# Kernel optimization log

Measured on AMD Instinct MI355X. Metric: run time of the kernel, lower is better.

## Reference

```python
import jax, jax.numpy as jnp
import numpy as np

B, S, D_IN, E = 64, 199, 1024, 256
INNER, K = 512, 4
NH_M, DH_M = 4, 128
NH_S, DH_S = 4, 64
FF_UP = 384
SLSTM_AT = (1, 4)


def layernorm(x, w, eps=1e-5):
    mu = x.mean(-1, keepdims=True)
    var = x.var(-1, keepdims=True)
    return (x - mu) * jax.lax.rsqrt(var + eps) * w


def mh_layernorm(h, w, eps=1e-5):
    # h: (B,S,NH,DH): normalize per head over DH, scale by w (NH*DH,)
    mu = h.mean(-1, keepdims=True)
    var = h.var(-1, keepdims=True)
    hn = (h - mu) * jax.lax.rsqrt(var + eps)
    b, s, nh, dh = h.shape
    return hn.reshape(b, s, nh * dh) * w


def causal_conv(x, w, b):
    # depthwise causal conv; x (B,S,C), w (C,K), b (C,)
    k = w.shape[-1]
    s = x.shape[1]
    xp = jnp.pad(x, ((0, 0), (k - 1, 0), (0, 0)))
    y = sum(xp[:, i:i + s, :] * w[:, i] for i in range(k))
    return y + b


def headwise(x, w):
    # block-diagonal linear (LinearHeadwiseExpand): x (B,S,H*d), w (H,o,d)
    b, s, _ = x.shape
    h, o, d = w.shape
    y = jnp.einsum('bshd,hod->bsho', x.reshape(b, s, h, d), w)
    return y.reshape(b, s, h * o)


def mlstm_parallel(q, k, v, ig, fg):
    # stabilized parallel mLSTM; q,k,v (B,NH,S,DH); ig,fg (B,NH,S)
    s, dh = q.shape[2], q.shape[3]
    logf = jax.nn.log_sigmoid(fg)
    lfc = jnp.cumsum(logf, axis=-1)
    lfc = jnp.concatenate([jnp.zeros_like(lfc[..., :1]), lfc], axis=-1)  # (B,NH,S+1)
    mat = lfc[..., :, None] - lfc[..., None, :]
    mask = jnp.tril(jnp.ones((s + 1, s + 1), dtype=bool))
    mat = jnp.where(mask, mat, -jnp.inf)
    logD = mat[..., 1:, 1:] + ig[..., None, :]            # (B,NH,S,S)
    maxD = jnp.max(logD, axis=-1, keepdims=True)
    Dm = jnp.exp(logD - maxD)
    qk = jnp.einsum('bnsd,bntd->bnst', q, k) / (dh ** 0.5)
    C = qk * Dm
    norm = jnp.maximum(jnp.abs(C.sum(-1, keepdims=True)), jnp.exp(-maxD))
    return jnp.einsum('bnst,bntd->bnsd', C / (norm + 1e-6), v)


def mlstm_layer(x, proj_up, conv_w, conv_b, q_w, k_w, v_w, ig_w, ig_b, fg_w, fg_b, skip, outnorm_w, proj_down):
    b, s, _ = x.shape
    xi = x @ proj_up                                      # (B,S,2*INNER)
    x_m, z = jnp.split(xi, 2, axis=-1)
    xca = jax.nn.silu(causal_conv(x_m, conv_w, conv_b))
    q = headwise(xca, q_w)
    k = headwise(xca, k_w)
    v = headwise(x_m, v_w)
    gate_in = jnp.concatenate([q, k, v], axis=-1)         # (B,S,3*INNER)
    ig = (gate_in @ ig_w.T + ig_b).transpose(0, 2, 1)     # (B,NH,S)
    fg = (gate_in @ fg_w.T + fg_b).transpose(0, 2, 1)
    qh = q.reshape(b, s, NH_M, DH_M).transpose(0, 2, 1, 3)
    kh = k.reshape(b, s, NH_M, DH_M).transpose(0, 2, 1, 3)
    vh = v.reshape(b, s, NH_M, DH_M).transpose(0, 2, 1, 3)
    h = mlstm_parallel(qh, kh, vh, ig, fg)                # (B,NH,S,DH)
    hn = mh_layernorm(h.transpose(0, 2, 1, 3), outnorm_w) # (B,S,INNER)
    h_state = (hn + skip * xca) * jax.nn.silu(z)
    return h_state @ proj_down


def slstm_layer(x, conv_w, conv_b, gate_w, rec_w, bias, gn_w):
    b, s, _ = x.shape
    xc = jax.nn.silu(causal_conv(x, conv_w, conv_b))
    xch = xc.reshape(b, s, NH_S, DH_S)
    xh = x.reshape(b, s, NH_S, DH_S)
    gi = jnp.einsum('bshd,hod->bsho', xch, gate_w[0])
    gf = jnp.einsum('bshd,hod->bsho', xch, gate_w[1])
    gz = jnp.einsum('bshd,hod->bsho', xh, gate_w[2])
    go = jnp.einsum('bshd,hod->bsho', xh, gate_w[3])
    Wx = jnp.stack([gi, gf, gz, go], axis=2)              # (B,S,4,NH,DH)

    def step(carry, wx):
        h, c, n, m = carry
        raw = wx + jnp.einsum('bhd,ghod->bgho', h, rec_w) + bias
        iraw, fraw, zraw, oraw = raw[:, 0], raw[:, 1], raw[:, 2], raw[:, 3]
        logfplusm = m + jax.nn.log_sigmoid(fraw)
        m_new = jnp.maximum(iraw, logfplusm)
        igate = jnp.exp(iraw - m_new)
        fgate = jnp.exp(logfplusm - m_new)
        c_new = fgate * c + igate * jnp.tanh(zraw)
        n_new = fgate * n + igate
        h_new = jax.nn.sigmoid(oraw) * (c_new / n_new)
        return (h_new, c_new, n_new, m_new), h_new

    z0 = jnp.zeros((b, NH_S, DH_S), x.dtype)
    _, ys = jax.lax.scan(step, (z0, z0, z0, z0), jnp.moveaxis(Wx, 1, 0))
    y = jnp.moveaxis(ys, 0, 1)                            # (B,S,NH,DH)
    return mh_layernorm(y, gn_w)


def gated_ffn(x, w_up, w_dn):
    gate, up = jnp.split(x @ w_up, 2, axis=-1)
    return (jax.nn.gelu(gate) * up) @ w_dn


def forward_fn(x, w_down, b_down, m_ln_w, m_proj_up, m_conv_w, m_conv_b, m_q_w, m_k_w, m_v_w,
               m_ig_w, m_ig_b, m_fg_w, m_fg_b, m_skip, m_outnorm_w, m_proj_down,
               s_ln_w, s_conv_w, s_conv_b, s_gate_w, s_rec_w, s_bias, s_gn_w, s_ln2_w,
               s_ffn_up, s_ffn_down, post_ln_w, w_emo, b_emo, w_sen, b_sen):
    h = x @ w_down + b_down                               # (B,S,E)
    mi = si = 0
    for blk in range(7):
        if blk in SLSTM_AT:
            h = h + slstm_layer(layernorm(h, s_ln_w[si]), s_conv_w[si], s_conv_b[si],
                                s_gate_w[si], s_rec_w[si], s_bias[si], s_gn_w[si])
            h = h + gated_ffn(layernorm(h, s_ln2_w[si]), s_ffn_up[si], s_ffn_down[si])
            si += 1
        else:
            h = h + mlstm_layer(layernorm(h, m_ln_w[mi]), m_proj_up[mi], m_conv_w[mi], m_conv_b[mi],
                                m_q_w[mi], m_k_w[mi], m_v_w[mi], m_ig_w[mi], m_ig_b[mi],
                                m_fg_w[mi], m_fg_b[mi], m_skip[mi], m_outnorm_w[mi], m_proj_down[mi])
            mi += 1
    h = jax.nn.selu(layernorm(h, post_ln_w))
    pooled = h.mean(axis=1)                               # (B,E)
    return pooled @ w_emo + b_emo, pooled @ w_sen + b_sen


def setup_inputs() -> dict:
    ks = iter(jax.random.split(jax.random.key(0), 40))
    def p(*shape, s=0.02):
        return jax.random.normal(next(ks), shape, dtype=jnp.float32) * s
    inp = dict(
        x=jax.random.normal(next(ks), (B, S, D_IN), dtype=jnp.float32),
        w_down=p(D_IN, E), b_down=jnp.zeros((E,), jnp.float32),
        m_ln_w=jnp.ones((5, E), jnp.float32),
        m_proj_up=p(5, E, 2 * INNER),
        m_conv_w=p(5, INNER, K), m_conv_b=jnp.zeros((5, INNER), jnp.float32),
        m_q_w=p(5, 128, 4, 4), m_k_w=p(5, 128, 4, 4), m_v_w=p(5, 128, 4, 4),
        m_ig_w=p(5, NH_M, 3 * INNER), m_ig_b=p(5, NH_M, s=0.1),
        m_fg_w=p(5, NH_M, 3 * INNER),
        m_fg_b=jnp.tile(jnp.linspace(3.0, 6.0, NH_M, dtype=jnp.float32), (5, 1)),
        m_skip=jnp.ones((5, INNER), jnp.float32),
        m_outnorm_w=jnp.ones((5, INNER), jnp.float32),
        m_proj_down=p(5, INNER, E),
        s_ln_w=jnp.ones((2, E), jnp.float32),
        s_conv_w=p(2, E, K), s_conv_b=jnp.zeros((2, E), jnp.float32),
        s_gate_w=p(2, 4, NH_S, DH_S, DH_S),
        s_rec_w=p(2, 4, NH_S, DH_S, DH_S),
        s_bias=jnp.zeros((2, 4, NH_S, DH_S), jnp.float32).at[:, 1].set(3.0),
        s_gn_w=jnp.ones((2, E), jnp.float32),
        s_ln2_w=jnp.ones((2, E), jnp.float32),
        s_ffn_up=p(2, E, 2 * FF_UP), s_ffn_down=p(2, FF_UP, E),
        post_ln_w=jnp.ones((E,), jnp.float32),
        w_emo=p(E, 7), b_emo=jnp.zeros((7,), jnp.float32),
        w_sen=p(E, 3), b_sen=jnp.zeros((3,), jnp.float32),
    )
    return inp


def reference(x, w_down, b_down, m_ln_w, m_proj_up, m_conv_w, m_conv_b, m_q_w, m_k_w, m_v_w,
              m_ig_w, m_ig_b, m_fg_w, m_fg_b, m_skip, m_outnorm_w, m_proj_down,
              s_ln_w, s_conv_w, s_conv_b, s_gate_w, s_rec_w, s_bias, s_gn_w, s_ln2_w,
              s_ffn_up, s_ffn_down, post_ln_w, w_emo, b_emo, w_sen, b_sen):
    return forward_fn(x, w_down, b_down, m_ln_w, m_proj_up, m_conv_w, m_conv_b, m_q_w, m_k_w, m_v_w,
                      m_ig_w, m_ig_b, m_fg_w, m_fg_b, m_skip, m_outnorm_w, m_proj_down,
                      s_ln_w, s_conv_w, s_conv_b, s_gate_w, s_rec_w, s_bias, s_gn_w, s_ln2_w,
                      s_ffn_up, s_ffn_down, post_ln_w, w_emo, b_emo, w_sen, b_sen)
```

## Files before the change

### kernel.cpp

```cpp
#include <hip/hip_runtime.h>
#include <hip/hip_bf16.h>
#include <math.h>


#define B_    64
#define S_    199
#define E_    256
#define NTOK  (B_*S_)
#define NQT   13

typedef __attribute__((ext_vector_type(8))) short short8;
typedef __attribute__((ext_vector_type(4))) float floatx4;
typedef unsigned short ushort_t;

__device__ __forceinline__ float sigmoidf_(float x) { return 1.f / (1.f + expf(-x)); }
__device__ __forceinline__ float siluf_(float x) { return x / (1.f + expf(-x)); }
__device__ __forceinline__ float logsigf_(float x) { return fminf(x, 0.f) - log1pf(expf(-fabsf(x))); }

__device__ __forceinline__ ushort_t f2b(float f) {
    union { float f; unsigned u; } v; v.f = f;
    unsigned r = (v.u + 0x7fffu + ((v.u >> 16) & 1u)) >> 16;
    return (ushort_t)r;
}
__device__ __forceinline__ float bf2f(ushort_t u) {
    union { unsigned u; float f; } v; v.u = ((unsigned)u) << 16;
    return v.f;
}
__device__ __forceinline__ void unp2(unsigned d, float& lo, float& hi) {
    union { unsigned u; float f; } a, b;
    a.u = d << 16; b.u = d & 0xffff0000u;
    lo = a.f; hi = b.f;
}

__global__ void cvt_bf(const float* __restrict__ in, ushort_t* __restrict__ out, int n4) {
    int i = blockIdx.x * 256 + threadIdx.x;
    if (i >= n4) return;
    float4 v = *(const float4*)&in[i * 4];
    union { ushort_t us[4]; uint2 u; } t;
    t.us[0] = f2b(v.x); t.us[1] = f2b(v.y); t.us[2] = f2b(v.z); t.us[3] = f2b(v.w);
    *(uint2*)&out[i * 4] = t.u;
}

__global__ void __launch_bounds__(256)
gemm_bf(const ushort_t* __restrict__ A, const ushort_t* __restrict__ Bw,
        const float* __restrict__ bias, float* __restrict__ C,
        int M, int K, int N, int accum) {
    __shared__ __align__(16) ushort_t As[64][40];
    __shared__ __align__(16) ushort_t Bs[128][40];
    int tid = threadIdx.x;
    int wave = tid >> 6, lane = tid & 63;
    int wm = wave >> 1, wn = wave & 1;
    int quad = lane >> 4, l16 = lane & 15;
    int m0 = blockIdx.y * 64, n0 = blockIdx.x * 128;
    floatx4 zero = {0.f, 0.f, 0.f, 0.f};
    floatx4 acc[2][4];
    #pragma unroll
    for (int i = 0; i < 2; i++)
        #pragma unroll
        for (int j = 0; j < 4; j++) acc[i][j] = zero;
    int ar = tid >> 2, ac = (tid & 3) * 8;
    int bn = tid & 127, bkg = (tid >> 7) * 16;
    for (int k0 = 0; k0 < K; k0 += 32) {
        *(uint4*)&As[ar][ac] = *(const uint4*)(A + (size_t)(m0 + ar) * K + k0 + ac);
        {
            const ushort_t* bp = Bw + (size_t)(k0 + bkg) * N + n0 + bn;
            union { ushort_t us[16]; uint4 v[2]; } t;
            #pragma unroll
            for (int i = 0; i < 16; i++) t.us[i] = bp[(size_t)i * N];
            *(uint4*)&Bs[bn][bkg] = t.v[0];
            *(uint4*)&Bs[bn][bkg + 8] = t.v[1];
        }
        __syncthreads();
        short8 af[2], bf[4];
        #pragma unroll
        for (int i = 0; i < 2; i++) af[i] = *(const short8*)&As[wm * 32 + i * 16 + l16][quad * 8];
        #pragma unroll
        for (int j = 0; j < 4; j++) bf[j] = *(const short8*)&Bs[wn * 64 + j * 16 + l16][quad * 8];
        #pragma unroll
        for (int i = 0; i < 2; i++)
            #pragma unroll
            for (int j = 0; j < 4; j++)
                acc[i][j] = __builtin_amdgcn_mfma_f32_16x16x32_bf16(af[i], bf[j], acc[i][j], 0, 0, 0);
        __syncthreads();
    }
    #pragma unroll
    for (int i = 0; i < 2; i++)
        #pragma unroll
        for (int j = 0; j < 4; j++)
            #pragma unroll
            for (int r = 0; r < 4; r++) {
                int row = m0 + wm * 32 + i * 16 + quad * 4 + r;
                int col = n0 + wn * 64 + j * 16 + l16;
                float o = acc[i][j][r];
                if (bias) o += bias[col];
                float* cp = &C[(size_t)row * N + col];
                if (accum) o += *cp;
                *cp = o;
            }
}

__global__ void __launch_bounds__(256)
gemm_mfma(const float* __restrict__ A, const float* __restrict__ Bw,
          const float* __restrict__ bias, float* __restrict__ C,
          int M, int K, int N, int accum) {
    __shared__ __align__(16) ushort_t As[64][40];
    __shared__ __align__(16) ushort_t Bs[64][40];
    int tid = threadIdx.x;
    int wave = tid >> 6, lane = tid & 63;
    int wm = wave >> 1, wn = wave & 1;
    int quad = lane >> 4, l16 = lane & 15;
    int m0 = blockIdx.y * 64, n0 = blockIdx.x * 64;
    floatx4 zero = {0.f, 0.f, 0.f, 0.f};
    floatx4 acc[2][2];
    acc[0][0] = zero; acc[0][1] = zero; acc[1][0] = zero; acc[1][1] = zero;
    int ar = tid >> 2, ac = (tid & 3) * 8;
    int bn = tid & 63, bk = (tid >> 6) * 8;
    for (int k0 = 0; k0 < K; k0 += 32) {
        {
            const float* ap = A + (size_t)(m0 + ar) * K + k0 + ac;
            union { ushort_t us[8]; uint4 v; } t;
            #pragma unroll
            for (int i = 0; i < 8; i++) t.us[i] = f2b(ap[i]);
            *(uint4*)&As[ar][ac] = t.v;
        }
        {
            const float* bp = Bw + (size_t)(k0 + bk) * N + n0 + bn;
            union { ushort_t us[8]; uint4 v; } t;
            #pragma unroll
            for (int i = 0; i < 8; i++) t.us[i] = f2b(bp[(size_t)i * N]);
            *(uint4*)&Bs[bn][bk] = t.v;
        }
        __syncthreads();
        short8 af[2], bf[2];
        #pragma unroll
        for (int i = 0; i < 2; i++) af[i] = *(const short8*)&As[wm * 32 + i * 16 + l16][quad * 8];
        #pragma unroll
        for (int j = 0; j < 2; j++) bf[j] = *(const short8*)&Bs[wn * 32 + j * 16 + l16][quad * 8];
        #pragma unroll
        for (int i = 0; i < 2; i++)
            #pragma unroll
            for (int j = 0; j < 2; j++)
                acc[i][j] = __builtin_amdgcn_mfma_f32_16x16x32_bf16(af[i], bf[j], acc[i][j], 0, 0, 0);
        __syncthreads();
    }
    #pragma unroll
    for (int i = 0; i < 2; i++)
        #pragma unroll
        for (int j = 0; j < 2; j++)
            #pragma unroll
            for (int r = 0; r < 4; r++) {
                int row = m0 + wm * 32 + i * 16 + quad * 4 + r;
                int col = n0 + wn * 32 + j * 16 + l16;
                float o = acc[i][j][r];
                if (bias) o += bias[col];
                float* cp = &C[(size_t)row * N + col];
                if (accum) o += *cp;
                *cp = o;
            }
}

__global__ void __launch_bounds__(256)
slstm_wx_mfma(const ushort_t* __restrict__ xc, const ushort_t* __restrict__ xln,
              const float* __restrict__ gw, float* __restrict__ Wx) {
    __shared__ __align__(16) ushort_t As[64][40];
    __shared__ __align__(16) ushort_t Bs[64][40];
    int gh = blockIdx.y; int g = gh >> 2, hh = gh & 3;
    const ushort_t* src = (g < 2) ? xc : xln;
    const float* w = gw + (size_t)gh * 4096;
    int tid = threadIdx.x;
    int wave = tid >> 6, lane = tid & 63;
    int wm = wave >> 1, wn = wave & 1;
    int quad = lane >> 4, l16 = lane & 15;
    int m0 = blockIdx.x * 64;
    floatx4 zero = {0.f, 0.f, 0.f, 0.f};
    floatx4 acc[2][2];
    acc[0][0] = zero; acc[0][1] = zero; acc[1][0] = zero; acc[1][1] = zero;
    int ar = tid >> 2, ac = (tid & 3) * 8;
    int bn = tid & 63, bk = (tid >> 6) * 8;
    #pragma unroll
    for (int kt = 0; kt < 2; kt++) {
        int k0 = kt * 32;
        *(uint4*)&As[ar][ac] = *(const uint4*)(src + (size_t)(m0 + ar) * 256 + hh * 64 + k0 + ac);
        {
            const float* bp = w + (size_t)bn * 64 + k0 + bk;
            union { ushort_t us[8]; uint4 v; } t;
            #pragma unroll
            for (int i = 0; i < 8; i++) t.us[i] = f2b(bp[i]);
            *(uint4*)&Bs[bn][bk] = t.v;
        }
        __syncthreads();
        short8 af[2], bf[2];
        #pragma unroll
        for (int i = 0; i < 2; i++) af[i] = *(const short8*)&As[wm * 32 + i * 16 + l16][quad * 8];
        #pragma unroll
        for (int j = 0; j < 2; j++) bf[j] = *(const short8*)&Bs[wn * 32 + j * 16 + l16][quad * 8];
        #pragma unroll
        for (int i = 0; i < 2; i++)
            #pragma unroll
            for (int j = 0; j < 2; j++)
                acc[i][j] = __builtin_amdgcn_mfma_f32_16x16x32_bf16(af[i], bf[j], acc[i][j], 0, 0, 0);
        __syncthreads();
    }
    #pragma unroll
    for (int i = 0; i < 2; i++)
        #pragma unroll
        for (int j = 0; j < 2; j++)
            #pragma unroll
            for (int r = 0; r < 4; r++) {
                int row = m0 + wm * 32 + i * 16 + quad * 4 + r;
                int col = wn * 32 + j * 16 + l16;
                Wx[(size_t)row * 1024 + g * 256 + hh * 64 + col] = acc[i][j][r];
            }
}

__global__ void __launch_bounds__(256)
layernorm256(const float* __restrict__ x, const float* __restrict__ w, ushort_t* __restrict__ y) {
    int n = blockIdx.x, t = threadIdx.x;
    float v = x[(size_t)n * 256 + t];
    float s = v, s2 = v * v;
    #pragma unroll
    for (int off = 32; off; off >>= 1) { s += __shfl_xor(s, off); s2 += __shfl_xor(s2, off); }
    __shared__ float ps[4], ps2[4];
    if ((t & 63) == 0) { ps[t >> 6] = s; ps2[t >> 6] = s2; }
    __syncthreads();
    float S = ps[0] + ps[1] + ps[2] + ps[3];
    float S2 = ps2[0] + ps2[1] + ps2[2] + ps2[3];
    float mu = S / 256.f, var = S2 / 256.f - mu * mu;
    y[(size_t)n * 256 + t] = f2b((v - mu) * rsqrtf(var + 1e-5f) * w[t]);
}

__global__ void __launch_bounds__(256)
postln_selu(const float* __restrict__ x, const float* __restrict__ w, float* __restrict__ y) {
    int n = blockIdx.x, t = threadIdx.x;
    float v = x[(size_t)n * 256 + t];
    float s = v, s2 = v * v;
    #pragma unroll
    for (int off = 32; off; off >>= 1) { s += __shfl_xor(s, off); s2 += __shfl_xor(s2, off); }
    __shared__ float ps[4], ps2[4];
    if ((t & 63) == 0) { ps[t >> 6] = s; ps2[t >> 6] = s2; }
    __syncthreads();
    float S = ps[0] + ps[1] + ps[2] + ps[3];
    float S2 = ps2[0] + ps2[1] + ps2[2] + ps2[3];
    float mu = S / 256.f, var = S2 / 256.f - mu * mu;
    float yn = (v - mu) * rsqrtf(var + 1e-5f) * w[t];
    y[(size_t)n * 256 + t] = 1.0507009873554805f * (yn > 0.f ? yn : 1.6732632423543772f * (expf(yn) - 1.f));
}

__global__ void __launch_bounds__(256)
fused_qkv(const float* __restrict__ xi, const float* __restrict__ cw,
          const float* __restrict__ cb,
          const float* __restrict__ qw, const float* __restrict__ kw,
          const float* __restrict__ vw,
          float* __restrict__ xca,
          ushort_t* __restrict__ q16, ushort_t* __restrict__ k16, ushort_t* __restrict__ v16) {
    int idx = blockIdx.x * 256 + threadIdx.x;
    if (idx >= NTOK * 128) return;
    int n = idx >> 7, hh = idx & 127;
    int b = n / S_, s = n - b * S_;
    int c0 = hh * 4;
    float4 hist[4];
    #pragma unroll
    for (int i = 0; i < 4; i++) {
        int sp = s - 3 + i;
        if (sp >= 0) hist[i] = *(const float4*)(xi + (size_t)(b * S_ + sp) * 1024 + c0);
        else hist[i] = (float4){0.f, 0.f, 0.f, 0.f};
    }
    float xm[4] = {hist[3].x, hist[3].y, hist[3].z, hist[3].w};
    float xc4[4];
    #pragma unroll
    for (int d = 0; d < 4; d++) {
        float y = cb[c0 + d];
        const float* cwp = cw + (c0 + d) * 4;
        y += hist[0].x * 0.f;
        float hv[4] = { d==0?hist[0].x:(d==1?hist[0].y:(d==2?hist[0].z:hist[0].w)),
                        d==0?hist[1].x:(d==1?hist[1].y:(d==2?hist[1].z:hist[1].w)),
                        d==0?hist[2].x:(d==1?hist[2].y:(d==2?hist[2].z:hist[2].w)),
                        xm[d] };
        #pragma unroll
        for (int i = 0; i < 4; i++) y += hv[i] * cwp[i];
        xc4[d] = siluf_(y);
    }
    *(float4*)(xca + (size_t)n * 512 + c0) = (float4){xc4[0], xc4[1], xc4[2], xc4[3]};
    union { ushort_t us[4]; uint2 u; } qo, ko, vo;
    #pragma unroll
    for (int o = 0; o < 4; o++) {
        const float* qp = qw + (c0 + o) * 4;
        const float* kp = kw + (c0 + o) * 4;
        const float* vp = vw + (c0 + o) * 4;
        float aq = 0.f, ak = 0.f, av = 0.f;
        #pragma unroll
        for (int d = 0; d < 4; d++) {
            aq += xc4[d] * qp[d];
            ak += xc4[d] * kp[d];
            av += xm[d] * vp[d];
        }
        qo.us[o] = f2b(aq); ko.us[o] = f2b(ak); vo.us[o] = f2b(av);
    }
    *(uint2*)(q16 + (size_t)n * 512 + c0) = qo.u;
    *(uint2*)(k16 + (size_t)n * 512 + c0) = ko.u;
    *(uint2*)(v16 + (size_t)n * 512 + c0) = vo.u;
}

__global__ void __launch_bounds__(256)
gates2(const ushort_t* __restrict__ qb, const ushort_t* __restrict__ kb, const ushort_t* __restrict__ vb,
       const float* __restrict__ igw, const float* __restrict__ igbias,
       const float* __restrict__ fgw, const float* __restrict__ fgbias,
       float* __restrict__ igo, float* __restrict__ fgo) {
    int n = blockIdx.x * 4 + (threadIdx.x >> 6);
    int lane = threadIdx.x & 63;
    uint4 q4 = *(const uint4*)(qb + (size_t)n * 512 + lane * 8);
    uint4 k4 = *(const uint4*)(kb + (size_t)n * 512 + lane * 8);
    uint4 v4 = *(const uint4*)(vb + (size_t)n * 512 + lane * 8);
    float q[8], k[8], v[8];
    unp2(q4.x, q[0], q[1]); unp2(q4.y, q[2], q[3]); unp2(q4.z, q[4], q[5]); unp2(q4.w, q[6], q[7]);
    unp2(k4.x, k[0], k[1]); unp2(k4.y, k[2], k[3]); unp2(k4.z, k[4], k[5]); unp2(k4.w, k[6], k[7]);
    unp2(v4.x, v[0], v[1]); unp2(v4.y, v[2], v[3]); unp2(v4.z, v[4], v[5]); unp2(v4.w, v[6], v[7]);
    float acc[8];
    #pragma unroll
    for (int hd = 0; hd < 4; hd++)
        #pragma unroll
        for (int wh = 0; wh < 2; wh++) {
            const float* w = (wh ? fgw : igw) + hd * 1536 + lane * 8;
            float a = 0.f;
            #pragma unroll
            for (int i = 0; i < 8; i++) a += q[i] * w[i];
            #pragma unroll
            for (int i = 0; i < 8; i++) a += k[i] * w[512 + i];
            #pragma unroll
            for (int i = 0; i < 8; i++) a += v[i] * w[1024 + i];
            acc[hd * 2 + wh] = a;
        }
    #pragma unroll
    for (int t = 0; t < 8; t++) {
        float a = acc[t];
        #pragma unroll
        for (int off = 32; off; off >>= 1) a += __shfl_xor(a, off);
        if (lane == 0) {
            int hd = t >> 1, wh = t & 1;
            a += (wh ? fgbias : igbias)[hd];
            (wh ? fgo : igo)[(size_t)n * 4 + hd] = a;
        }
    }
}

__global__ void __launch_bounds__(256)
mlstm_cumsum(const float* __restrict__ fgo, const float* __restrict__ igo,
             float* __restrict__ lfc, float* __restrict__ Mx) {
    int bh = blockIdx.x * 4 + (threadIdx.x >> 6);
    int lane = threadIdx.x & 63;
    int b = bh >> 2, h = bh & 3;
    float v[4]; float lsum = 0.f;
    #pragma unroll
    for (int i = 0; i < 4; i++) {
        int s = lane * 4 + i;
        float f = (s < S_) ? fgo[(size_t)(b * S_ + s) * 4 + h] : 0.f;
        lsum += logsigf_(f);
        v[i] = lsum;
    }
    float x = lsum;
    #pragma unroll
    for (int off = 1; off < 64; off <<= 1) {
        float y = __shfl_up(x, off);
        if (lane >= off) x += y;
    }
    float excl = x - lsum;
    float lf1[4];
    #pragma unroll
    for (int i = 0; i < 4; i++) lf1[i] = excl + v[i];
    if (lane == 0) lfc[bh * (S_ + 1)] = 0.f;
    #pragma unroll
    for (int i = 0; i < 4; i++) {
        int s = lane * 4 + i;
        if (s < S_) lfc[bh * (S_ + 1) + s + 1] = lf1[i];
    }
    float gm[4]; float lmax = -1e30f;
    #pragma unroll
    for (int i = 0; i < 4; i++) {
        int s = lane * 4 + i;
        float ig_ = (s < S_) ? igo[(size_t)(b * S_ + s) * 4 + h] : -1e30f;
        float gg = ig_ - lf1[i];
        lmax = fmaxf(lmax, gg);
        gm[i] = lmax;
    }
    float xm = lmax;
    #pragma unroll
    for (int off = 1; off < 64; off <<= 1) {
        float y = __shfl_up(xm, off);
        if (lane >= off) xm = fmaxf(xm, y);
    }
    float exclm = __shfl_up(xm, 1);
    if (lane == 0) exclm = -1e30f;
    #pragma unroll
    for (int i = 0; i < 4; i++) {
        int s = lane * 4 + i;
        if (s < S_) Mx[bh * S_ + s] = fmaxf(exclm, gm[i]);
    }
}

__global__ void __launch_bounds__(256, 1)
mlstm_attn_mfma(const ushort_t* __restrict__ qb, const ushort_t* __restrict__ kb, const ushort_t* __restrict__ vb,
                const float* __restrict__ igb, const float* __restrict__ lfc, const float* __restrict__ Mx,
                float* __restrict__ outb) {
    __shared__ __align__(16) ushort_t Kb[64 * 136];
    __shared__ __align__(16) ushort_t Vt[128 * 72];
    __shared__ __align__(16) ushort_t Pw[4][16 * 72];
    __shared__ float gv[208], lfv[208], mxv[208];
    int bh = blockIdx.x; int b = bh >> 2, h = bh & 3;
    int tid = threadIdx.x, wave = tid >> 6, lane = tid & 63;
    int quad = lane >> 4, l16 = lane & 15;
    if (tid < 208) {
        if (tid < S_) {
            float lf1 = lfc[bh * (S_ + 1) + tid + 1];
            gv[tid] = igb[(size_t)(b * S_ + tid) * 4 + h] - lf1;
            lfv[tid] = lf1;
            mxv[tid] = Mx[bh * S_ + tid];
        } else { gv[tid] = 0.f; lfv[tid] = 0.f; mxv[tid] = 0.f; }
    }
    floatx4 zero = {0.f, 0.f, 0.f, 0.f};
    float rs[4][4];
    floatx4 accv[4][8];
    #pragma unroll
    for (int qi = 0; qi < 4; qi++) {
        #pragma unroll
        for (int r = 0; r < 4; r++) rs[qi][r] = 0.f;
        #pragma unroll
        for (int dt = 0; dt < 8; dt++) accv[qi][dt] = zero;
    }
    const float scale = 0.08838834764831845f;
    int trow = tid >> 4, d0 = (tid & 15) * 8;
    for (int c = 0; c < 4; c++) {
        __syncthreads();
        #pragma unroll
        for (int i = 0; i < 4; i++) {
            int tl = trow + 16 * i;
            int t = c * 64 + tl;
            union { ushort_t us[8]; uint4 v; } kk, vv;
            if (t < S_) {
                kk.v = *(const uint4*)(kb + (size_t)(b * S_ + t) * 512 + h * 128 + d0);
                vv.v = *(const uint4*)(vb + (size_t)(b * S_ + t) * 512 + h * 128 + d0);
            } else {
                kk.v = (uint4){0, 0, 0, 0};
                vv.v = (uint4){0, 0, 0, 0};
            }
            *(uint4*)&Kb[tl * 136 + d0] = kk.v;
            #pragma unroll
            for (int ii = 0; ii < 8; ii++) Vt[(d0 + ii) * 72 + tl] = vv.us[ii];
        }
        __syncthreads();
        for (int qi = 0; qi < 4; qi++) {
            int qt = wave + 4 * qi;
            if (qt >= NQT || qt < 4 * c) continue;
            uint4 z4 = {0, 0, 0, 0};
            for (int z = lane; z < 144; z += 64) ((uint4*)Pw[wave])[z] = z4;
            int srow = qt * 16 + l16;
            const ushort_t* qp = qb + (size_t)(b * S_ + min(srow, S_ - 1)) * 512 + h * 128 + quad * 8;
            short8 af[4];
            #pragma unroll
            for (int ks = 0; ks < 4; ks++) af[ks] = *(const short8*)(qp + 32 * ks);
            int ktmax_l = min(qt, 4 * c + 3) - 4 * c;
            for (int ktl = 0; ktl <= ktmax_l; ktl++) {
                floatx4 acc = zero;
                #pragma unroll
                for (int ks = 0; ks < 4; ks++) {
                    short8 bf = *(const short8*)&Kb[(ktl * 16 + l16) * 136 + quad * 8 + 32 * ks];
                    acc = __builtin_amdgcn_mfma_f32_16x16x32_bf16(af[ks], bf, acc, 0, 0, 0);
                }
                int tcol = c * 64 + ktl * 16 + l16;
                float gt = gv[tcol];
                #pragma unroll
                for (int r = 0; r < 4; r++) {
                    int s = qt * 16 + quad * 4 + r;
                    bool valid = (tcol <= s) && (tcol < S_);
                    float w = valid ? expf(gt - mxv[s]) : 0.f;
                    float p = acc[r] * scale * w;
                    rs[qi][r] += p;
                    Pw[wave][(quad * 4 + r) * 72 + ktl * 16 + l16] = f2b(p);
                }
            }
            #pragma unroll
            for (int dt = 0; dt < 8; dt++) {
                floatx4 a = accv[qi][dt];
                #pragma unroll
                for (int ks = 0; ks < 2; ks++) {
                    short8 ap = *(const short8*)&Pw[wave][l16 * 72 + quad * 8 + 32 * ks];
                    short8 bp = *(const short8*)&Vt[(dt * 16 + l16) * 72 + quad * 8 + 32 * ks];
                    a = __builtin_amdgcn_mfma_f32_16x16x32_bf16(ap, bp, a, 0, 0, 0);
                }
                accv[qi][dt] = a;
            }
        }
    }
    for (int qi = 0; qi < 4; qi++) {
        int qt = wave + 4 * qi;
        if (qt >= NQT) continue;
        float nrm[4];
        #pragma unroll
        for (int r = 0; r < 4; r++) {
            float v = rs[qi][r];
            v += __shfl_xor(v, 1); v += __shfl_xor(v, 2);
            v += __shfl_xor(v, 4); v += __shfl_xor(v, 8);
            int s = qt * 16 + quad * 4 + r;
            nrm[r] = fmaxf(fabsf(v), expf(-(lfv[s] + mxv[s]))) + 1e-6f;
        }
        #pragma unroll
        for (int dt = 0; dt < 8; dt++)
            #pragma unroll
            for (int r = 0; r < 4; r++) {
                int s = qt * 16 + quad * 4 + r;
                if (s < S_)
                    outb[(size_t)(b * S_ + s) * 512 + h * 128 + dt * 16 + l16] = accv[qi][dt][r] / nrm[r];
            }
    }
}

__global__ void __launch_bounds__(512)
mhln_hstate(const float* __restrict__ hatt, const float* __restrict__ w,
            const float* __restrict__ xca, const float* __restrict__ xi,
            const float* __restrict__ skip, ushort_t* __restrict__ out16) {
    int n = blockIdx.x, t = threadIdx.x;
    float v = hatt[(size_t)n * 512 + t];
    float s = v, s2 = v * v;
    #pragma unroll
    for (int off = 32; off; off >>= 1) { s += __shfl_xor(s, off); s2 += __shfl_xor(s2, off); }
    __shared__ float ps[8], ps2[8];
    if ((t & 63) == 0) { ps[t >> 6] = s; ps2[t >> 6] = s2; }
    __syncthreads();
    int hd = t >> 7;
    float S = ps[hd * 2] + ps[hd * 2 + 1], S2 = ps2[hd * 2] + ps2[hd * 2 + 1];
    float mu = S / 128.f, var = S2 / 128.f - mu * mu;
    float hn = (v - mu) * rsqrtf(var + 1e-5f) * w[t];
    float z = xi[(size_t)n * 1024 + 512 + t];
    out16[(size_t)n * 512 + t] = f2b((hn + skip[t] * xca[(size_t)n * 512 + t]) * siluf_(z));
}

__global__ void conv_silu_s(const ushort_t* __restrict__ xln, const float* __restrict__ cw,
                            const float* __restrict__ cb, ushort_t* __restrict__ xc) {
    int idx = blockIdx.x * blockDim.x + threadIdx.x;
    if (idx >= NTOK * 256) return;
    int n = idx >> 8, c = idx & 255;
    int b = n / S_, s = n - b * S_;
    float y = cb[c];
    #pragma unroll
    for (int i = 0; i < 4; i++) {
        int sp = s - 3 + i;
        if (sp >= 0) y += bf2f(xln[(size_t)(b * S_ + sp) * 256 + c]) * cw[c * 4 + i];
    }
    xc[idx] = f2b(siluf_(y));
}

__global__ void __launch_bounds__(512)
slstm_rec(const float* __restrict__ Wx, const float* __restrict__ rw,
          const float* __restrict__ bias, float* __restrict__ ys) {
    __shared__ __align__(16) float wl[512 * 36];
    __shared__ __align__(16) float hs[64];
    __shared__ float raws[4][64];
    int b = blockIdx.x >> 2, h = blockIdx.x & 3;
    int tid = threadIdx.x;
    int g = tid >> 7, o = (tid >> 1) & 63, kh = tid & 1;
    const float* wp = rw + (size_t)(((g * 4 + h) * 64 + o)) * 64 + kh * 32;
    float* myrow = wl + tid * 36;
    #pragma unroll
    for (int i = 0; i < 8; i++) *(float4*)&myrow[i * 4] = *(const float4*)&wp[i * 4];
    float bi = bias[(g * 4 + h) * 64 + o];
    if (tid < 64) hs[tid] = 0.f;
    float c_ = 0.f, n_ = 0.f, m_ = 0.f;
    size_t wxbase = (size_t)(b * S_) * 1024 + g * 256 + h * 64 + o;
    float wx_cur = Wx[wxbase];
    __syncthreads();
    for (int s = 0; s < S_; s++) {
        float wx_next = (s + 1 < S_) ? Wx[wxbase + (size_t)(s + 1) * 1024] : 0.f;
        float a0 = 0.f, a1 = 0.f, a2 = 0.f, a3 = 0.f;
        #pragma unroll
        for (int d4 = 0; d4 < 8; d4++) {
            float4 wv = *(const float4*)&myrow[d4 * 4];
            float4 hv = *(const float4*)&hs[kh * 32 + d4 * 4];
            a0 += hv.x * wv.x;
            a1 += hv.y * wv.y;
            a2 += hv.z * wv.z;
            a3 += hv.w * wv.w;
        }
        float a = (a0 + a1) + (a2 + a3);
        a += __shfl_xor(a, 1);
        if (kh == 0) raws[g][o] = a + wx_cur + bi;
        __syncthreads();
        float ir = raws[0][o], fr = raws[1][o], zr = raws[2][o], orr = raws[3][o];
        float lfpm = m_ + logsigf_(fr);
        float mn = fmaxf(ir, lfpm);
        float ig = expf(ir - mn), fg = expf(lfpm - mn);
        c_ = fg * c_ + ig * tanhf(zr);
        n_ = fg * n_ + ig;
        m_ = mn;
        float hn = sigmoidf_(orr) * (c_ / n_);
        if (g == 0 && kh == 0) {
            hs[o] = hn;
            ys[(size_t)(b * S_ + s) * 256 + h * 64 + o] = hn;
        }
        __syncthreads();
        wx_cur = wx_next;
    }
}

__global__ void __launch_bounds__(256)
mhln_s_resid(const float* __restrict__ ys, const float* __restrict__ w, float* __restrict__ h) {
    int n = blockIdx.x, t = threadIdx.x;
    float v = ys[(size_t)n * 256 + t];
    float s = v, s2 = v * v;
    #pragma unroll
    for (int off = 32; off; off >>= 1) { s += __shfl_xor(s, off); s2 += __shfl_xor(s2, off); }
    float mu = s / 64.f, var = s2 / 64.f - mu * mu;
    h[(size_t)n * 256 + t] += (v - mu) * rsqrtf(var + 1e-5f) * w[t];
}

__global__ void ffn_act(const float* __restrict__ up, ushort_t* __restrict__ act) {
    int idx = blockIdx.x * blockDim.x + threadIdx.x;
    if (idx >= NTOK * 384) return;
    int n = idx / 384, j = idx - n * 384;
    float g = up[(size_t)n * 768 + j], u = up[(size_t)n * 768 + 384 + j];
    float t = tanhf(0.7978845608028654f * (g + 0.044715f * g * g * g));
    act[idx] = f2b(0.5f * g * (1.f + t) * u);
}

__global__ void pool_k(const float* __restrict__ a, float* __restrict__ pooled) {
    int b = blockIdx.x, e = threadIdx.x;
    float s = 0.f;
    for (int t = 0; t < S_; t++) s += a[(size_t)(b * S_ + t) * 256 + e];
    pooled[b * 256 + e] = s / (float)S_;
}

__global__ void heads_k(const float* __restrict__ pooled,
                        const float* __restrict__ we, const float* __restrict__ be,
                        const float* __restrict__ ws, const float* __restrict__ bs,
                        float* __restrict__ out) {
    int i = blockIdx.x * blockDim.x + threadIdx.x;
    if (i < B_ * 7) {
        int b = i / 7, o = i - b * 7;
        float a = be[o];
        for (int e = 0; e < 256; e++) a += pooled[b * 256 + e] * we[e * 7 + o];
        out[b * 7 + o] = a;
    } else if (i < B_ * 7 + B_ * 3) {
        int j = i - B_ * 7;
        int b = j / 3, o = j - b * 3;
        float a = bs[o];
        for (int e = 0; e < 256; e++) a += pooled[b * 256 + e] * ws[e * 3 + o];
        out[B_ * 7 + b * 3 + o] = a;
    }
}

extern "C" void kernel_launch(void* const* d_in, const int* in_sizes, int n_in,
                              void* d_out, int out_size, void* d_ws, size_t ws_size,
                              hipStream_t stream) {
    (void)in_sizes; (void)n_in; (void)out_size; (void)ws_size;
    const float* x          = (const float*)d_in[0];
    const float* w_down     = (const float*)d_in[1];
    const float* b_down     = (const float*)d_in[2];
    const float* m_ln_w     = (const float*)d_in[3];
    const float* m_proj_up  = (const float*)d_in[4];
    const float* m_conv_w   = (const float*)d_in[5];
    const float* m_conv_b   = (const float*)d_in[6];
    const float* m_q_w      = (const float*)d_in[7];
    const float* m_k_w      = (const float*)d_in[8];
    const float* m_v_w      = (const float*)d_in[9];
    const float* m_ig_w     = (const float*)d_in[10];
    const float* m_ig_b     = (const float*)d_in[11];
    const float* m_fg_w     = (const float*)d_in[12];
    const float* m_fg_b     = (const float*)d_in[13];
    const float* m_skip     = (const float*)d_in[14];
    const float* m_outnorm  = (const float*)d_in[15];
    const float* m_proj_dn  = (const float*)d_in[16];
    const float* s_ln_w     = (const float*)d_in[17];
    const float* s_conv_w   = (const float*)d_in[18];
    const float* s_conv_b   = (const float*)d_in[19];
    const float* s_gate_w   = (const float*)d_in[20];
    const float* s_rec_w    = (const float*)d_in[21];
    const float* s_bias     = (const float*)d_in[22];
    const float* s_gn_w     = (const float*)d_in[23];
    const float* s_ln2_w    = (const float*)d_in[24];
    const float* s_ffn_up   = (const float*)d_in[25];
    const float* s_ffn_dn   = (const float*)d_in[26];
    const float* post_ln_w  = (const float*)d_in[27];
    const float* w_emo      = (const float*)d_in[28];
    const float* b_emo      = (const float*)d_in[29];
    const float* w_sen      = (const float*)d_in[30];
    const float* b_sen      = (const float*)d_in[31];

    float* W    = (float*)d_ws;
    float* h    = W;
    float* lnb  = h    + (size_t)NTOK * 256;
    float* big0 = lnb  + (size_t)NTOK * 256;
    float* xca  = big0 + (size_t)NTOK * 1024;
    float* qb   = xca  + (size_t)NTOK * 512;
    float* kb   = qb   + (size_t)NTOK * 512;
    float* vb   = kb   + (size_t)NTOK * 512;
    float* hatt = vb   + (size_t)NTOK * 512;
    float* igo  = hatt + (size_t)NTOK * 512;
    float* fgo  = igo  + (size_t)NTOK * 4;
    float* lfcb = fgo  + (size_t)NTOK * 4;
    float* Mxb  = lfcb + (size_t)256 * (S_ + 1);
    float* pooled = Mxb + (size_t)256 * S_;
    ushort_t* lnb16 = (ushort_t*)lnb;
    ushort_t* qb16  = (ushort_t*)qb;
    ushort_t* kb16  = (ushort_t*)kb;
    ushort_t* vb16  = (ushort_t*)vb;
    ushort_t* hat16 = qb16 + (size_t)NTOK * 512;
    ushort_t* xc16  = (ushort_t*)(vb16 + (size_t)NTOK * 512);
    ushort_t* wpk   = (ushort_t*)(pooled + 64 * 256);
    ushort_t* wp_pu = wpk;
    ushort_t* wp_pd = wp_pu + 5 * 262144;
    ushort_t* wp_fu = wp_pd + 5 * 131072;
    ushort_t* wp_fd = wp_fu + 2 * 196608;

    cvt_bf<<<(5 * 262144 / 4 + 255) / 256, 256, 0, stream>>>(m_proj_up, wp_pu, 5 * 262144 / 4);
    cvt_bf<<<(5 * 131072 / 4 + 255) / 256, 256, 0, stream>>>(m_proj_dn, wp_pd, 5 * 131072 / 4);
    cvt_bf<<<(2 * 196608 / 4 + 255) / 256, 256, 0, stream>>>(s_ffn_up, wp_fu, 2 * 196608 / 4);
    cvt_bf<<<(2 * 98304 / 4 + 255) / 256, 256, 0, stream>>>(s_ffn_dn, wp_fd, 2 * 98304 / 4);

    gemm_mfma<<<dim3(256 / 64, NTOK / 64), 256, 0, stream>>>(x, w_down, b_down, h, NTOK, 1024, 256, 0);

    int mi = 0, si = 0;
    for (int blk = 0; blk < 7; blk++) {
        if (blk == 1 || blk == 4) {
            layernorm256<<<NTOK, 256, 0, stream>>>(h, s_ln_w + si * 256, lnb16);
            conv_silu_s<<<(NTOK * 256 + 255) / 256, 256, 0, stream>>>(lnb16, s_conv_w + si * 1024, s_conv_b + si * 256, xc16);
            slstm_wx_mfma<<<dim3(NTOK / 64, 16), 256, 0, stream>>>(xc16, lnb16, s_gate_w + (size_t)si * 65536, big0);
            slstm_rec<<<256, 512, 0, stream>>>(big0, s_rec_w + (size_t)si * 65536, s_bias + si * 1024, hatt);
            mhln_s_resid<<<NTOK, 256, 0, stream>>>(hatt, s_gn_w + si * 256, h);
            layernorm256<<<NTOK, 256, 0, stream>>>(h, s_ln2_w + si * 256, lnb16);
            gemm_bf<<<dim3(768 / 128, NTOK / 64), 256, 0, stream>>>(lnb16, wp_fu + (size_t)si * 196608, nullptr, big0, NTOK, 256, 768, 0);
            ffn_act<<<(NTOK * 384 + 255) / 256, 256, 0, stream>>>(big0, hat16);
            gemm_bf<<<dim3(256 / 128, NTOK / 64), 256, 0, stream>>>(hat16, wp_fd + (size_t)si * 98304, nullptr, h, NTOK, 384, 256, 1);
            si++;
        } else {
            layernorm256<<<NTOK, 256, 0, stream>>>(h, m_ln_w + mi * 256, lnb16);
            gemm_bf<<<dim3(1024 / 128, NTOK / 64), 256, 0, stream>>>(lnb16, wp_pu + (size_t)mi * 262144, nullptr, big0, NTOK, 256, 1024, 0);
            fused_qkv<<<(NTOK * 128 + 255) / 256, 256, 0, stream>>>(big0, m_conv_w + mi * 2048, m_conv_b + mi * 512,
                                                                    m_q_w + mi * 2048, m_k_w + mi * 2048, m_v_w + mi * 2048,
                                                                    xca, qb16, kb16, vb16);
            gates2<<<NTOK / 4, 256, 0, stream>>>(qb16, kb16, vb16, m_ig_w + mi * 6144, m_ig_b + mi * 4,
                                                 m_fg_w + mi * 6144, m_fg_b + mi * 4, igo, fgo);
            mlstm_cumsum<<<64, 256, 0, stream>>>(fgo, igo, lfcb, Mxb);
            mlstm_attn_mfma<<<256, 256, 0, stream>>>(qb16, kb16, vb16, igo, lfcb, Mxb, hatt);
            mhln_hstate<<<NTOK, 512, 0, stream>>>(hatt, m_outnorm + mi * 512, xca, big0, m_skip + mi * 512, hat16);
            gemm_bf<<<dim3(256 / 128, NTOK / 64), 256, 0, stream>>>(hat16, wp_pd + (size_t)mi * 131072, nullptr, h, NTOK, 512, 256, 1);
            mi++;
        }
    }

    postln_selu<<<NTOK, 256, 0, stream>>>(h, post_ln_w, xca);
    pool_k<<<B_, 256, 0, stream>>>(xca, pooled);
    heads_k<<<3, 256, 0, stream>>>(pooled, w_emo, b_emo, w_sen, b_sen, (float*)d_out);
}
```

Before: 1.989 ms.

## Merge weight conversions, keep sLSTM recurrent weights in registers, fuse post-norms

```diff
diff --git a/kernel.cpp b/kernel.cpp
--- a/kernel.cpp
+++ b/kernel.cpp
@@ -32,13 +32,21 @@
     lo = a.f; hi = b.f;
 }
 
-__global__ void cvt_bf(const float* __restrict__ in, ushort_t* __restrict__ out, int n4) {
+__global__ void cvt_all(const float* __restrict__ pu, const float* __restrict__ pd,
+                        const float* __restrict__ fu, const float* __restrict__ fd,
+                        ushort_t* __restrict__ out, int n4) {
     int i = blockIdx.x * 256 + threadIdx.x;
     if (i >= n4) return;
-    float4 v = *(const float4*)&in[i * 4];
+    int e = i * 4;
+    const float* src;
+    if (e < 1310720)      src = pu + e;
+    else if (e < 1966080) src = pd + (e - 1310720);
+    else if (e < 2359296) src = fu + (e - 1966080);
+    else                  src = fd + (e - 2359296);
+    float4 v = *(const float4*)src;
     union { ushort_t us[4]; uint2 u; } t;
     t.us[0] = f2b(v.x); t.us[1] = f2b(v.y); t.us[2] = f2b(v.z); t.us[3] = f2b(v.w);
-    *(uint2*)&out[i * 4] = t.u;
+    *(uint2*)&out[e] = t.u;
 }
 
 __global__ void __launch_bounds__(256)
@@ -271,7 +279,6 @@
     for (int d = 0; d < 4; d++) {
         float y = cb[c0 + d];
         const float* cwp = cw + (c0 + d) * 4;
-        y += hist[0].x * 0.f;
         float hv[4] = { d==0?hist[0].x:(d==1?hist[0].y:(d==2?hist[0].z:hist[0].w)),
                         d==0?hist[1].x:(d==1?hist[1].y:(d==2?hist[1].z:hist[1].w)),
                         d==0?hist[2].x:(d==1?hist[2].y:(d==2?hist[2].z:hist[2].w)),
@@ -551,16 +558,17 @@
 __global__ void __launch_bounds__(512)
 slstm_rec(const float* __restrict__ Wx, const float* __restrict__ rw,
           const float* __restrict__ bias, float* __restrict__ ys) {
-    __shared__ __align__(16) float wl[512 * 36];
     __shared__ __align__(16) float hs[64];
     __shared__ float raws[4][64];
     int b = blockIdx.x >> 2, h = blockIdx.x & 3;
     int tid = threadIdx.x;
     int g = tid >> 7, o = (tid >> 1) & 63, kh = tid & 1;
+    float w[32];
     const float* wp = rw + (size_t)(((g * 4 + h) * 64 + o)) * 64 + kh * 32;
-    float* myrow = wl + tid * 36;
-    #pragma unroll
-    for (int i = 0; i < 8; i++) *(float4*)&myrow[i * 4] = *(const float4*)&wp[i * 4];
+    #pragma unroll
+    for (int d = 0; d < 32; d++) w[d] = wp[d];
+    #pragma unroll
+    for (int d = 0; d < 32; d++) asm volatile("" : "+v"(w[d]));
     float bi = bias[(g * 4 + h) * 64 + o];
     if (tid < 64) hs[tid] = 0.f;
     float c_ = 0.f, n_ = 0.f, m_ = 0.f;
@@ -572,12 +580,11 @@
         float a0 = 0.f, a1 = 0.f, a2 = 0.f, a3 = 0.f;
         #pragma unroll
         for (int d4 = 0; d4 < 8; d4++) {
-            float4 wv = *(const float4*)&myrow[d4 * 4];
             float4 hv = *(const float4*)&hs[kh * 32 + d4 * 4];
-            a0 += hv.x * wv.x;
-            a1 += hv.y * wv.y;
-            a2 += hv.z * wv.z;
-            a3 += hv.w * wv.w;
+            a0 += hv.x * w[4 * d4 + 0];
+            a1 += hv.y * w[4 * d4 + 1];
+            a2 += hv.z * w[4 * d4 + 2];
+            a3 += hv.w * w[4 * d4 + 3];
         }
         float a = (a0 + a1) + (a2 + a3);
         a += __shfl_xor(a, 1);
@@ -601,14 +608,27 @@
 }
 
 __global__ void __launch_bounds__(256)
-mhln_s_resid(const float* __restrict__ ys, const float* __restrict__ w, float* __restrict__ h) {
+slstm_post(const float* __restrict__ ys, const float* __restrict__ gn_w,
+           float* __restrict__ h, const float* __restrict__ ln2_w,
+           ushort_t* __restrict__ ln16) {
     int n = blockIdx.x, t = threadIdx.x;
     float v = ys[(size_t)n * 256 + t];
     float s = v, s2 = v * v;
     #pragma unroll
     for (int off = 32; off; off >>= 1) { s += __shfl_xor(s, off); s2 += __shfl_xor(s2, off); }
     float mu = s / 64.f, var = s2 / 64.f - mu * mu;
-    h[(size_t)n * 256 + t] += (v - mu) * rsqrtf(var + 1e-5f) * w[t];
+    float hv = h[(size_t)n * 256 + t] + (v - mu) * rsqrtf(var + 1e-5f) * gn_w[t];
+    h[(size_t)n * 256 + t] = hv;
+    float S = hv, S2 = hv * hv;
+    #pragma unroll
+    for (int off = 32; off; off >>= 1) { S += __shfl_xor(S, off); S2 += __shfl_xor(S2, off); }
+    __shared__ float ps[4], ps2[4];
+    if ((t & 63) == 0) { ps[t >> 6] = S; ps2[t >> 6] = S2; }
+    __syncthreads();
+    float St = ps[0] + ps[1] + ps[2] + ps[3];
+    float S2t = ps2[0] + ps2[1] + ps2[2] + ps2[3];
+    float mu2 = St / 256.f, var2 = S2t / 256.f - mu2 * mu2;
+    ln16[(size_t)n * 256 + t] = f2b((hv - mu2) * rsqrtf(var2 + 1e-5f) * ln2_w[t]);
 }
 
 __global__ void ffn_act(const float* __restrict__ up, ushort_t* __restrict__ act) {
@@ -709,10 +729,7 @@
     ushort_t* wp_fu = wp_pd + 5 * 131072;
     ushort_t* wp_fd = wp_fu + 2 * 196608;
 
-    cvt_bf<<<(5 * 262144 / 4 + 255) / 256, 256, 0, stream>>>(m_proj_up, wp_pu, 5 * 262144 / 4);
-    cvt_bf<<<(5 * 131072 / 4 + 255) / 256, 256, 0, stream>>>(m_proj_dn, wp_pd, 5 * 131072 / 4);
-    cvt_bf<<<(2 * 196608 / 4 + 255) / 256, 256, 0, stream>>>(s_ffn_up, wp_fu, 2 * 196608 / 4);
-    cvt_bf<<<(2 * 98304 / 4 + 255) / 256, 256, 0, stream>>>(s_ffn_dn, wp_fd, 2 * 98304 / 4);
+    cvt_all<<<(638976 + 255) / 256, 256, 0, stream>>>(m_proj_up, m_proj_dn, s_ffn_up, s_ffn_dn, wpk, 638976);
 
     gemm_mfma<<<dim3(256 / 64, NTOK / 64), 256, 0, stream>>>(x, w_down, b_down, h, NTOK, 1024, 256, 0);
 
@@ -723,8 +740,7 @@
             conv_silu_s<<<(NTOK * 256 + 255) / 256, 256, 0, stream>>>(lnb16, s_conv_w + si * 1024, s_conv_b + si * 256, xc16);
             slstm_wx_mfma<<<dim3(NTOK / 64, 16), 256, 0, stream>>>(xc16, lnb16, s_gate_w + (size_t)si * 65536, big0);
             slstm_rec<<<256, 512, 0, stream>>>(big0, s_rec_w + (size_t)si * 65536, s_bias + si * 1024, hatt);
-            mhln_s_resid<<<NTOK, 256, 0, stream>>>(hatt, s_gn_w + si * 256, h);
-            layernorm256<<<NTOK, 256, 0, stream>>>(h, s_ln2_w + si * 256, lnb16);
+            slstm_post<<<NTOK, 256, 0, stream>>>(hatt, s_gn_w + si * 256, h, s_ln2_w + si * 256, lnb16);
             gemm_bf<<<dim3(768 / 128, NTOK / 64), 256, 0, stream>>>(lnb16, wp_fu + (size_t)si * 196608, nullptr, big0, NTOK, 256, 768, 0);
             ffn_act<<<(NTOK * 384 + 255) / 256, 256, 0, stream>>>(big0, hat16);
             gemm_bf<<<dim3(256 / 128, NTOK / 64), 256, 0, stream>>>(hat16, wp_fd + (size_t)si * 98304, nullptr, h, NTOK, 384, 256, 1);
```

New measurement: 1.919 ms. -3.5%, faster.
